# Performance work log

Measured on AMD Instinct MI355X. Metric: run time of the kernel, lower is better.

## Reference

```python
import jax, jax.numpy as jnp
import numpy as np

NUM_HEADS = 12

def setup_inputs() -> dict:
    key = jax.random.key(0)
    ks = jax.random.split(key, 9)
    B, N, C = 4, 1024, 768
    hd = C // NUM_HEADS  # 64
    return {
        "x": jax.random.normal(ks[0], (B, N, C), dtype=jnp.float32),
        "prev_attn": jax.random.uniform(ks[1], (B, NUM_HEADS, N, N), dtype=jnp.float32) / N,
        "qkv_w": jax.random.normal(ks[2], (3 * C, C), dtype=jnp.float32) * 0.02,
        "proj_w": jax.random.normal(ks[3], (C, C), dtype=jnp.float32) * 0.02,
        "proj_b": jax.random.normal(ks[4], (C,), dtype=jnp.float32) * 0.02,
        "bp_w1": jax.random.normal(ks[5], (hd // 2, 2 * hd), dtype=jnp.float32) * 0.02,
        "bp_b1": jax.random.normal(ks[6], (hd // 2,), dtype=jnp.float32) * 0.02,
        "bp_w2": jax.random.normal(ks[7], (3, hd // 2), dtype=jnp.float32) * 0.02,
        "bp_b2": jax.random.normal(ks[8], (3,), dtype=jnp.float32) * 0.02,
    }

def reference(x, prev_attn, qkv_w, proj_w, proj_b, bp_w1, bp_b1, bp_w2, bp_b2):
    B, N, C = x.shape
    H = NUM_HEADS
    hd = C // H
    scale = hd ** -0.5
    # qkv projection: [B,N,3C] -> [3,B,H,N,hd]
    qkv = (x @ qkv_w.T).reshape(B, N, 3, H, hd).transpose(2, 0, 3, 1, 4)
    q, k, v = qkv[0], qkv[1], qkv[2]
    # scaled dot-product scores [B,H,N,N]
    attn_logits = jnp.einsum('bhnd,bhmd->bhnm', q, k) * scale
    cur_attn = jax.nn.softmax(attn_logits, axis=-1)
    # per-(b,h,n) bias MLP on concat(q,k): [B,H,N,2*hd] -> [B,H,N,3]
    qk = jnp.concatenate((q, k), axis=-1)
    h1 = jax.nn.relu(jnp.einsum('bhnd,od->bhno', qk, bp_w1) + bp_b1)
    bias = jnp.abs(jnp.einsum('bhno,po->bhnp', h1, bp_w2) + bp_b2)  # [B,H,N,3]
    # blend current attention, previous attention, and uniform term
    attn = (cur_attn * (1.0 + bias[..., 0:1])
            + prev_attn * bias[..., 1:2]
            - bias[..., 2:3] / N)
    out = jnp.einsum('bhnm,bhmd->bhnd', attn, v)  # [B,H,N,hd]
    out = out.transpose(0, 2, 1, 3).reshape(B, N, C)
    out = out @ proj_w.T + proj_b
    return (out, cur_attn)
```

## Files before the change

kernel.cpp:

```cpp
#include <hip/hip_runtime.h>

typedef __bf16 bf16_t;
typedef __bf16 bf16x8 __attribute__((ext_vector_type(8)));
typedef __bf16 bf16x4 __attribute__((ext_vector_type(4)));
typedef float f32x4 __attribute__((ext_vector_type(4)));

static constexpr int Bb = 4, Hh = 12, Nn = 1024, Cc = 768, HD = 64;
static constexpr int OUT0 = Bb * Nn * Cc;

__global__ __launch_bounds__(256) void convert_all(
    const float* __restrict__ x, const float* __restrict__ qw, const float* __restrict__ pw,
    bf16_t* __restrict__ xb, bf16_t* __restrict__ qwb, bf16_t* __restrict__ pwb) {
  const int NX = (Bb * Nn * Cc) / 4;
  const int NQ = (3 * Cc * Cc) / 4;
  int i = blockIdx.x * 256 + threadIdx.x;
  const float4* src;
  bf16_t* dst;
  int off;
  if (i < NX) { src = (const float4*)x; dst = xb; off = i; }
  else if (i < NX + NQ) { src = (const float4*)qw; dst = qwb; off = i - NX; }
  else { src = (const float4*)pw; dst = pwb; off = i - NX - NQ; }
  float4 v = src[off];
  bf16x4 o;
  o[0] = (bf16_t)v.x; o[1] = (bf16_t)v.y; o[2] = (bf16_t)v.z; o[3] = (bf16_t)v.w;
  *(bf16x4*)(dst + (size_t)off * 4) = o;
}

template <int MODE>
__global__ __launch_bounds__(256) void gemm_bt(
    const bf16_t* __restrict__ A, const bf16_t* __restrict__ Bm, int N, int K,
    bf16_t* __restrict__ q_bf, bf16_t* __restrict__ k_bf, bf16_t* __restrict__ vT_bf,
    float* __restrict__ outF, const float* __restrict__ bias) {
  __shared__ bf16_t As[128 * 40];
  __shared__ bf16_t Bs[128 * 40];
  const int tid = threadIdx.x;
  const int lane = tid & 63;
  const int w = tid >> 6;
  const int wr = w >> 1, wc = w & 1;
  const int g = lane >> 4, r = lane & 15;
  const int ntiles = N >> 7;
  const int m0 = (blockIdx.x / ntiles) << 7;
  const int n0 = (blockIdx.x % ntiles) << 7;

  const f32x4 fz = {0.f, 0.f, 0.f, 0.f};
  f32x4 acc[4][4];
#pragma unroll
  for (int i = 0; i < 4; i++)
#pragma unroll
    for (int j = 0; j < 4; j++) acc[i][j] = fz;

  for (int k0 = 0; k0 < K; k0 += 32) {
#pragma unroll
    for (int p = 0; p < 2; p++) {
      int idx = tid + (p << 8);
      int row = idx >> 2;
      int kof = (idx & 3) << 3;
      *(bf16x8*)&As[row * 40 + kof] = *(const bf16x8*)&A[(size_t)(m0 + row) * K + k0 + kof];
      *(bf16x8*)&Bs[row * 40 + kof] = *(const bf16x8*)&Bm[(size_t)(n0 + row) * K + k0 + kof];
    }
    __syncthreads();
    bf16x8 af[4], bfv[4];
#pragma unroll
    for (int i = 0; i < 4; i++) af[i] = *(const bf16x8*)&As[(wr * 64 + i * 16 + r) * 40 + g * 8];
#pragma unroll
    for (int j = 0; j < 4; j++) bfv[j] = *(const bf16x8*)&Bs[(wc * 64 + j * 16 + r) * 40 + g * 8];
#pragma unroll
    for (int i = 0; i < 4; i++)
#pragma unroll
      for (int j = 0; j < 4; j++)
        acc[i][j] = __builtin_amdgcn_mfma_f32_16x16x32_bf16(af[i], bfv[j], acc[i][j], 0, 0, 0);
    __syncthreads();
  }

#pragma unroll
  for (int i = 0; i < 4; i++) {
#pragma unroll
    for (int j = 0; j < 4; j++) {
      int c = n0 + wc * 64 + j * 16 + r;
#pragma unroll
      for (int e = 0; e < 4; e++) {
        int mrow = m0 + wr * 64 + i * 16 + g * 4 + e;
        float val = acc[i][j][e];
        if constexpr (MODE == 0) {
          int which = c / 768;
          int cc = c - which * 768;
          int h = cc >> 6, d = cc & 63;
          int b = mrow >> 10, n = mrow & 1023;
          size_t bh = (size_t)(b * Hh + h);
          if (which == 0)      q_bf[(bh * Nn + n) * HD + d] = (bf16_t)val;
          else if (which == 1) k_bf[(bh * Nn + n) * HD + d] = (bf16_t)val;
          else                 vT_bf[(bh * HD + d) * Nn + n] = (bf16_t)val;
        } else {
          outF[(size_t)mrow * N + c] = val + bias[c];
        }
      }
    }
  }
}

__global__ __launch_bounds__(256) void bias_mlp(
    const bf16_t* __restrict__ qb, const bf16_t* __restrict__ kb,
    const float* __restrict__ w1, const float* __restrict__ b1,
    const float* __restrict__ w2, const float* __restrict__ b2,
    float* __restrict__ bias4) {
  __shared__ float w1s[32 * 129];
  __shared__ float qks[8][128];
  __shared__ float h1s[8][32];
  const int t = threadIdx.x;
#pragma unroll
  for (int p = 0; p < 16; p++) {
    int idx = p * 256 + t;
    w1s[(idx >> 7) * 129 + (idx & 127)] = w1[idx];
  }
  const int rl = t >> 5, u = t & 31;
  const int rowg = blockIdx.x * 8 + rl;
  {
    int i4 = u * 4;
    const bf16_t* src = (i4 < 64) ? (qb + (size_t)rowg * HD + i4)
                                  : (kb + (size_t)rowg * HD + (i4 - 64));
    bf16x4 vv = *(const bf16x4*)src;
#pragma unroll
    for (int z = 0; z < 4; z++) qks[rl][i4 + z] = (float)vv[z];
  }
  __syncthreads();
  float accv = b1[u];
#pragma unroll 8
  for (int i = 0; i < 128; i++) accv += qks[rl][i] * w1s[u * 129 + i];
  h1s[rl][u] = fmaxf(accv, 0.f);
  __syncthreads();
  if (u < 4) {
    float outv = 0.f;
    if (u < 3) {
      float s = b2[u];
#pragma unroll
      for (int j = 0; j < 32; j++) s += w2[u * 32 + j] * h1s[rl][j];
      float v = fabsf(s);
      outv = (u == 0) ? (1.f + v) : ((u == 1) ? v : -v * (1.f / (float)Nn));
    }
    bias4[(size_t)rowg * 4 + u] = outv;
  }
}

__global__ __launch_bounds__(256) void attn_fused(
    const bf16_t* __restrict__ qb, const bf16_t* __restrict__ kb,
    const bf16_t* __restrict__ vT, const float* __restrict__ prev,
    const float* __restrict__ bias4, float* __restrict__ cur,
    bf16_t* __restrict__ oh) {
  __shared__ bf16_t Pb[16 * 1024];
  __shared__ float redmax[16][4];
  __shared__ float redsum[16][4];
  const int bid = blockIdx.x;
  const int bh = bid >> 6, mt = bid & 63;
  const int tid = threadIdx.x;
  const int lane = tid & 63, w = tid >> 6;
  const int g = lane >> 4, r = lane & 15;
  const int row0 = mt << 4;

  const bf16_t* qp = qb + ((size_t)bh * Nn + row0) * HD;
  const bf16_t* kp = kb + (size_t)bh * Nn * HD;
  bf16x8 a0 = *(const bf16x8*)&qp[r * HD + g * 8];
  bf16x8 a1 = *(const bf16x8*)&qp[r * HD + g * 8 + 32];
  const f32x4 fz = {0.f, 0.f, 0.f, 0.f};
  f32x4 acc[16];
#pragma unroll
  for (int t = 0; t < 16; t++) {
    int col = (w << 8) + (t << 4) + r;
    bf16x8 b0 = *(const bf16x8*)&kp[(size_t)col * HD + g * 8];
    bf16x8 b1 = *(const bf16x8*)&kp[(size_t)col * HD + g * 8 + 32];
    f32x4 z = __builtin_amdgcn_mfma_f32_16x16x32_bf16(a0, b0, fz, 0, 0, 0);
    acc[t] = __builtin_amdgcn_mfma_f32_16x16x32_bf16(a1, b1, z, 0, 0, 0);
  }
  const float scale = 0.125f;
  float mj[4] = {-3.0e38f, -3.0e38f, -3.0e38f, -3.0e38f};
#pragma unroll
  for (int t = 0; t < 16; t++)
#pragma unroll
    for (int e = 0; e < 4; e++) {
      acc[t][e] *= scale;
      mj[e] = fmaxf(mj[e], acc[t][e]);
    }
#pragma unroll
  for (int s = 1; s < 16; s <<= 1)
#pragma unroll
    for (int e = 0; e < 4; e++) mj[e] = fmaxf(mj[e], __shfl_xor(mj[e], s, 64));
  if (r == 0) {
#pragma unroll
    for (int e = 0; e < 4; e++) redmax[g * 4 + e][w] = mj[e];
  }
  __syncthreads();
  float rm[4];
#pragma unroll
  for (int e = 0; e < 4; e++) {
    float v = fmaxf(redmax[g * 4 + e][0], redmax[g * 4 + e][1]);
    rm[e] = fmaxf(v, fmaxf(redmax[g * 4 + e][2], redmax[g * 4 + e][3]));
  }
  float sj[4] = {0.f, 0.f, 0.f, 0.f};
#pragma unroll
  for (int t = 0; t < 16; t++)
#pragma unroll
    for (int e = 0; e < 4; e++) {
      float ev = __expf(acc[t][e] - rm[e]);
      acc[t][e] = ev;
      sj[e] += ev;
    }
#pragma unroll
  for (int s = 1; s < 16; s <<= 1)
#pragma unroll
    for (int e = 0; e < 4; e++) sj[e] += __shfl_xor(sj[e], s, 64);
  if (r == 0) {
#pragma unroll
    for (int e = 0; e < 4; e++) redsum[g * 4 + e][w] = sj[e];
  }
  __syncthreads();
  float inv[4];
#pragma unroll
  for (int e = 0; e < 4; e++)
    inv[e] = 1.f / (redsum[g * 4 + e][0] + redsum[g * 4 + e][1] +
                    redsum[g * 4 + e][2] + redsum[g * 4 + e][3]);
  float* op = cur + (size_t)bh * Nn * Nn;
#pragma unroll
  for (int t = 0; t < 16; t++) {
    int col = (w << 8) + (t << 4) + r;
#pragma unroll
    for (int e = 0; e < 4; e++) {
      float p = acc[t][e] * inv[e];
      int row = g * 4 + e;
      op[(size_t)(row0 + row) * Nn + col] = p;
      Pb[row * 1024 + (col ^ ((row & 7) << 3))] = (bf16_t)p;
    }
  }
  __syncthreads();

  const float* pp = prev + (size_t)bh * Nn * Nn + (size_t)row0 * Nn;
  const float* bp = bias4 + ((size_t)(bh << 10) + row0) * 4;
#pragma unroll
  for (int i = 0; i < 16; i++) {
    float4 pv = *(const float4*)&pp[(size_t)i * Nn + tid * 4];
    float4 bv = *(const float4*)&bp[i * 4];
    int ci = (tid * 4) ^ ((i & 7) << 3);
    bf16x4 pbv = *(bf16x4*)&Pb[i * 1024 + ci];
    bf16x4 nb;
    nb[0] = (bf16_t)(bv.x * (float)pbv[0] + bv.y * pv.x + bv.z);
    nb[1] = (bf16_t)(bv.x * (float)pbv[1] + bv.y * pv.y + bv.z);
    nb[2] = (bf16_t)(bv.x * (float)pbv[2] + bv.y * pv.z + bv.z);
    nb[3] = (bf16_t)(bv.x * (float)pbv[3] + bv.y * pv.w + bv.z);
    *(bf16x4*)&Pb[i * 1024 + ci] = nb;
  }
  __syncthreads();

  const bf16_t* vp = vT + ((size_t)bh * HD + (w << 4) + r) * Nn;
  f32x4 c0 = fz, c1 = fz, c2 = fz, c3 = fz;
#pragma unroll
  for (int ks = 0; ks < 8; ks++) {
    int kA = ks * 32;
    bf16x8 afA = *(bf16x8*)&Pb[r * 1024 + ((kA + g * 8) ^ ((r & 7) << 3))];
    bf16x8 afB = *(bf16x8*)&Pb[r * 1024 + ((256 + kA + g * 8) ^ ((r & 7) << 3))];
    bf16x8 afC = *(bf16x8*)&Pb[r * 1024 + ((512 + kA + g * 8) ^ ((r & 7) << 3))];
    bf16x8 afD = *(bf16x8*)&Pb[r * 1024 + ((768 + kA + g * 8) ^ ((r & 7) << 3))];
    bf16x8 bA = *(const bf16x8*)&vp[kA + g * 8];
    bf16x8 bB = *(const bf16x8*)&vp[256 + kA + g * 8];
    bf16x8 bC = *(const bf16x8*)&vp[512 + kA + g * 8];
    bf16x8 bD = *(const bf16x8*)&vp[768 + kA + g * 8];
    c0 = __builtin_amdgcn_mfma_f32_16x16x32_bf16(afA, bA, c0, 0, 0, 0);
    c1 = __builtin_amdgcn_mfma_f32_16x16x32_bf16(afB, bB, c1, 0, 0, 0);
    c2 = __builtin_amdgcn_mfma_f32_16x16x32_bf16(afC, bC, c2, 0, 0, 0);
    c3 = __builtin_amdgcn_mfma_f32_16x16x32_bf16(afD, bD, c3, 0, 0, 0);
  }
  f32x4 osum = (c0 + c1) + (c2 + c3);
  const int b = bh / Hh, h = bh % Hh;
#pragma unroll
  for (int e = 0; e < 4; e++) {
    int nrow = row0 + g * 4 + e;
    oh[((size_t)(b * Nn + nrow)) * Cc + h * HD + (w << 4) + r] = (bf16_t)osum[e];
  }
}

extern "C" void kernel_launch(void* const* d_in, const int* in_sizes, int n_in,
                              void* d_out, int out_size, void* d_ws, size_t ws_size,
                              hipStream_t stream) {
  const float* x      = (const float*)d_in[0];
  const float* prev   = (const float*)d_in[1];
  const float* qkv_w  = (const float*)d_in[2];
  const float* proj_w = (const float*)d_in[3];
  const float* proj_b = (const float*)d_in[4];
  const float* bp_w1  = (const float*)d_in[5];
  const float* bp_b1  = (const float*)d_in[6];
  const float* bp_w2  = (const float*)d_in[7];
  const float* bp_w2b = (const float*)d_in[8];

  float* out0 = (float*)d_out;
  float* cur  = out0 + OUT0;

  char* ws = (char*)d_ws;
  bf16_t* xb    = (bf16_t*)(ws + 0);
  bf16_t* qwb   = (bf16_t*)(ws + 6291456);
  bf16_t* pwb   = (bf16_t*)(ws + 9830400);
  bf16_t* qbf   = (bf16_t*)(ws + 11010048);
  bf16_t* kbf   = (bf16_t*)(ws + 17301504);
  bf16_t* vtb   = (bf16_t*)(ws + 23592960);
  float*  bias4 = (float*)(ws + 29884416);
  bf16_t* ohb   = (bf16_t*)(ws + 30670848);
  if (ws_size < 36962304) return;

  convert_all<<<5376, 256, 0, stream>>>(x, qkv_w, proj_w, xb, qwb, pwb);
  gemm_bt<0><<<(4096 / 128) * (2304 / 128), 256, 0, stream>>>(
      xb, qwb, 2304, 768, qbf, kbf, vtb, nullptr, nullptr);
  bias_mlp<<<49152 / 8, 256, 0, stream>>>(qbf, kbf, bp_w1, bp_b1, bp_w2, bp_w2b, bias4);
  attn_fused<<<48 * 64, 256, 0, stream>>>(qbf, kbf, vtb, prev, bias4, cur, ohb);
  gemm_bt<1><<<(4096 / 128) * (768 / 128), 256, 0, stream>>>(
      ohb, pwb, 768, 768, nullptr, nullptr, nullptr, out0, proj_b);
}
```

Baseline: 249.1 us.

## Use direct global-to-LDS loads in QKV GEMM and restructure attention softmax stores

```diff
diff --git a/kernel.cpp b/kernel.cpp
--- a/kernel.cpp
+++ b/kernel.cpp
@@ -7,6 +7,11 @@
 
 static constexpr int Bb = 4, Hh = 12, Nn = 1024, Cc = 768, HD = 64;
 static constexpr int OUT0 = Bb * Nn * Cc;
+
+#define GLD16(gp, lp)                                                       \
+  __builtin_amdgcn_global_load_lds(                                         \
+      (const __attribute__((address_space(1))) unsigned int*)(gp),          \
+      (__attribute__((address_space(3))) unsigned int*)(lp), 16, 0, 0)
 
 __global__ __launch_bounds__(256) void convert_all(
     const float* __restrict__ x, const float* __restrict__ qw, const float* __restrict__ pw,
@@ -26,10 +31,73 @@
   *(bf16x4*)(dst + (size_t)off * 4) = o;
 }
 
+__global__ __launch_bounds__(256) void gemm_qkv(
+    const bf16_t* __restrict__ A, const bf16_t* __restrict__ Bm,
+    bf16_t* __restrict__ q_bf, bf16_t* __restrict__ k_bf, bf16_t* __restrict__ vT_bf) {
+  __shared__ bf16_t As[128 * 32];
+  __shared__ bf16_t Bs[128 * 32];
+  const int tid = threadIdx.x;
+  const int lane = tid & 63;
+  const int w = tid >> 6;
+  const int wr = w >> 1, wc = w & 1;
+  const int g = lane >> 4, r = lane & 15;
+  const int m0 = (blockIdx.x / 18) << 7;
+  const int n0 = (blockIdx.x % 18) << 7;
+
+  const f32x4 fz = {0.f, 0.f, 0.f, 0.f};
+  f32x4 acc[4][4];
+#pragma unroll
+  for (int i = 0; i < 4; i++)
+#pragma unroll
+    for (int j = 0; j < 4; j++) acc[i][j] = fz;
+
+  for (int k0 = 0; k0 < 768; k0 += 32) {
+#pragma unroll
+    for (int c = 0; c < 2; c++) {
+      int row = w * 32 + c * 16 + (lane >> 2);
+      int kof = (lane & 3) << 3;
+      GLD16(&A[(size_t)(m0 + row) * 768 + k0 + kof], (char*)As + w * 2048 + c * 1024);
+      GLD16(&Bm[(size_t)(n0 + row) * 768 + k0 + kof], (char*)Bs + w * 2048 + c * 1024);
+    }
+    __syncthreads();
+    bf16x8 af[4], bfv[4];
+#pragma unroll
+    for (int i = 0; i < 4; i++) af[i] = *(const bf16x8*)&As[(wr * 64 + i * 16 + r) * 32 + g * 8];
+#pragma unroll
+    for (int j = 0; j < 4; j++) bfv[j] = *(const bf16x8*)&Bs[(wc * 64 + j * 16 + r) * 32 + g * 8];
+#pragma unroll
+    for (int i = 0; i < 4; i++)
+#pragma unroll
+      for (int j = 0; j < 4; j++)
+        acc[i][j] = __builtin_amdgcn_mfma_f32_16x16x32_bf16(af[i], bfv[j], acc[i][j], 0, 0, 0);
+    __syncthreads();
+  }
+
+#pragma unroll
+  for (int i = 0; i < 4; i++) {
+#pragma unroll
+    for (int j = 0; j < 4; j++) {
+      int c = n0 + wc * 64 + j * 16 + r;
+#pragma unroll
+      for (int e = 0; e < 4; e++) {
+        int mrow = m0 + wr * 64 + i * 16 + g * 4 + e;
+        float val = acc[i][j][e];
+        int which = c / 768;
+        int cc = c - which * 768;
+        int h = cc >> 6, d = cc & 63;
+        int b = mrow >> 10, n = mrow & 1023;
+        size_t bh = (size_t)(b * Hh + h);
+        if (which == 0)      q_bf[(bh * Nn + n) * HD + d] = (bf16_t)val;
+        else if (which == 1) k_bf[(bh * Nn + n) * HD + d] = (bf16_t)val;
+        else                 vT_bf[(bh * HD + d) * Nn + n] = (bf16_t)val;
+      }
+    }
+  }
+}
+
 template <int MODE>
 __global__ __launch_bounds__(256) void gemm_bt(
     const bf16_t* __restrict__ A, const bf16_t* __restrict__ Bm, int N, int K,
-    bf16_t* __restrict__ q_bf, bf16_t* __restrict__ k_bf, bf16_t* __restrict__ vT_bf,
     float* __restrict__ outF, const float* __restrict__ bias) {
   __shared__ bf16_t As[128 * 40];
   __shared__ bf16_t Bs[128 * 40];
@@ -80,19 +148,7 @@
 #pragma unroll
       for (int e = 0; e < 4; e++) {
         int mrow = m0 + wr * 64 + i * 16 + g * 4 + e;
-        float val = acc[i][j][e];
-        if constexpr (MODE == 0) {
-          int which = c / 768;
-          int cc = c - which * 768;
-          int h = cc >> 6, d = cc & 63;
-          int b = mrow >> 10, n = mrow & 1023;
-          size_t bh = (size_t)(b * Hh + h);
-          if (which == 0)      q_bf[(bh * Nn + n) * HD + d] = (bf16_t)val;
-          else if (which == 1) k_bf[(bh * Nn + n) * HD + d] = (bf16_t)val;
-          else                 vT_bf[(bh * HD + d) * Nn + n] = (bf16_t)val;
-        } else {
-          outF[(size_t)mrow * N + c] = val + bias[c];
-        }
+        outF[(size_t)mrow * N + c] = acc[i][j][e] + bias[c];
       }
     }
   }
@@ -141,16 +197,17 @@
   }
 }
 
-__global__ __launch_bounds__(256) void attn_fused(
+__global__ __launch_bounds__(256, 4) void attn_fused(
     const bf16_t* __restrict__ qb, const bf16_t* __restrict__ kb,
     const bf16_t* __restrict__ vT, const float* __restrict__ prev,
     const float* __restrict__ bias4, float* __restrict__ cur,
     bf16_t* __restrict__ oh) {
-  __shared__ bf16_t Pb[16 * 1024];
+  __shared__ char Plb[16 * 2048];
   __shared__ float redmax[16][4];
   __shared__ float redsum[16][4];
   const int bid = blockIdx.x;
-  const int bh = bid >> 6, mt = bid & 63;
+  const int tile = (bid & 7) * 384 + (bid >> 3);
+  const int bh = tile >> 6, mt = tile & 63;
   const int tid = threadIdx.x;
   const int lane = tid & 63, w = tid >> 6;
   const int g = lane >> 4, r = lane & 15;
@@ -217,54 +274,64 @@
   for (int e = 0; e < 4; e++)
     inv[e] = 1.f / (redsum[g * 4 + e][0] + redsum[g * 4 + e][1] +
                     redsum[g * 4 + e][2] + redsum[g * 4 + e][3]);
-  float* op = cur + (size_t)bh * Nn * Nn;
 #pragma unroll
   for (int t = 0; t < 16; t++) {
     int col = (w << 8) + (t << 4) + r;
 #pragma unroll
     for (int e = 0; e < 4; e++) {
-      float p = acc[t][e] * inv[e];
       int row = g * 4 + e;
-      op[(size_t)(row0 + row) * Nn + col] = p;
-      Pb[row * 1024 + (col ^ ((row & 7) << 3))] = (bf16_t)p;
-    }
-  }
-  __syncthreads();
-
-  const float* pp = prev + (size_t)bh * Nn * Nn + (size_t)row0 * Nn;
+      int off = (row * 2048 + col * 2) ^ ((row & 7) << 4);
+      *(bf16_t*)(Plb + off) = (bf16_t)(acc[t][e] * inv[e]);
+    }
+  }
+  __syncthreads();
+
+  const int c4 = tid << 2;
+  const float* pp = prev + (size_t)bh * Nn * Nn + (size_t)row0 * Nn + c4;
+  float* cp = cur + (size_t)bh * Nn * Nn + (size_t)row0 * Nn + c4;
   const float* bp = bias4 + ((size_t)(bh << 10) + row0) * 4;
 #pragma unroll
-  for (int i = 0; i < 16; i++) {
-    float4 pv = *(const float4*)&pp[(size_t)i * Nn + tid * 4];
-    float4 bv = *(const float4*)&bp[i * 4];
-    int ci = (tid * 4) ^ ((i & 7) << 3);
-    bf16x4 pbv = *(bf16x4*)&Pb[i * 1024 + ci];
-    bf16x4 nb;
-    nb[0] = (bf16_t)(bv.x * (float)pbv[0] + bv.y * pv.x + bv.z);
-    nb[1] = (bf16_t)(bv.x * (float)pbv[1] + bv.y * pv.y + bv.z);
-    nb[2] = (bf16_t)(bv.x * (float)pbv[2] + bv.y * pv.z + bv.z);
-    nb[3] = (bf16_t)(bv.x * (float)pbv[3] + bv.y * pv.w + bv.z);
-    *(bf16x4*)&Pb[i * 1024 + ci] = nb;
-  }
-  __syncthreads();
-
-  const bf16_t* vp = vT + ((size_t)bh * HD + (w << 4) + r) * Nn;
+  for (int half = 0; half < 2; half++) {
+    float4 pv[8];
+#pragma unroll
+    for (int i = 0; i < 8; i++)
+      pv[i] = *(const float4*)&pp[(size_t)(half * 8 + i) * Nn];
+#pragma unroll
+    for (int i = 0; i < 8; i++) {
+      int row = half * 8 + i;
+      int off = (row * 2048 + c4 * 2) ^ ((row & 7) << 4);
+      bf16x4 p4 = *(const bf16x4*)(Plb + off);
+      float4 pf;
+      pf.x = (float)p4[0]; pf.y = (float)p4[1]; pf.z = (float)p4[2]; pf.w = (float)p4[3];
+      *(float4*)&cp[(size_t)row * Nn] = pf;
+      float4 bv = *(const float4*)&bp[row * 4];
+      bf16x4 nb;
+      nb[0] = (bf16_t)(bv.x * pf.x + bv.y * pv[i].x + bv.z);
+      nb[1] = (bf16_t)(bv.x * pf.y + bv.y * pv[i].y + bv.z);
+      nb[2] = (bf16_t)(bv.x * pf.z + bv.y * pv[i].z + bv.z);
+      nb[3] = (bf16_t)(bv.x * pf.w + bv.y * pv[i].w + bv.z);
+      *(bf16x4*)(Plb + off) = nb;
+    }
+  }
+  __syncthreads();
+
+  const bf16_t* vrow = vT + (size_t)bh * HD * Nn + (size_t)((w << 4) + r) * Nn;
   f32x4 c0 = fz, c1 = fz, c2 = fz, c3 = fz;
 #pragma unroll
   for (int ks = 0; ks < 8; ks++) {
-    int kA = ks * 32;
-    bf16x8 afA = *(bf16x8*)&Pb[r * 1024 + ((kA + g * 8) ^ ((r & 7) << 3))];
-    bf16x8 afB = *(bf16x8*)&Pb[r * 1024 + ((256 + kA + g * 8) ^ ((r & 7) << 3))];
-    bf16x8 afC = *(bf16x8*)&Pb[r * 1024 + ((512 + kA + g * 8) ^ ((r & 7) << 3))];
-    bf16x8 afD = *(bf16x8*)&Pb[r * 1024 + ((768 + kA + g * 8) ^ ((r & 7) << 3))];
-    bf16x8 bA = *(const bf16x8*)&vp[kA + g * 8];
-    bf16x8 bB = *(const bf16x8*)&vp[256 + kA + g * 8];
-    bf16x8 bC = *(const bf16x8*)&vp[512 + kA + g * 8];
-    bf16x8 bD = *(const bf16x8*)&vp[768 + kA + g * 8];
-    c0 = __builtin_amdgcn_mfma_f32_16x16x32_bf16(afA, bA, c0, 0, 0, 0);
-    c1 = __builtin_amdgcn_mfma_f32_16x16x32_bf16(afB, bB, c1, 0, 0, 0);
-    c2 = __builtin_amdgcn_mfma_f32_16x16x32_bf16(afC, bC, c2, 0, 0, 0);
-    c3 = __builtin_amdgcn_mfma_f32_16x16x32_bf16(afD, bD, c3, 0, 0, 0);
+    int kA = ks << 5;
+    bf16x8 pA = *(const bf16x8*)(Plb + ((r * 2048 + (kA + g * 8) * 2) ^ ((r & 7) << 4)));
+    bf16x8 pB = *(const bf16x8*)(Plb + ((r * 2048 + (256 + kA + g * 8) * 2) ^ ((r & 7) << 4)));
+    bf16x8 pC = *(const bf16x8*)(Plb + ((r * 2048 + (512 + kA + g * 8) * 2) ^ ((r & 7) << 4)));
+    bf16x8 pD = *(const bf16x8*)(Plb + ((r * 2048 + (768 + kA + g * 8) * 2) ^ ((r & 7) << 4)));
+    bf16x8 vA = *(const bf16x8*)&vrow[kA + g * 8];
+    bf16x8 vB = *(const bf16x8*)&vrow[256 + kA + g * 8];
+    bf16x8 vC = *(const bf16x8*)&vrow[512 + kA + g * 8];
+    bf16x8 vD = *(const bf16x8*)&vrow[768 + kA + g * 8];
+    c0 = __builtin_amdgcn_mfma_f32_16x16x32_bf16(pA, vA, c0, 0, 0, 0);
+    c1 = __builtin_amdgcn_mfma_f32_16x16x32_bf16(pB, vB, c1, 0, 0, 0);
+    c2 = __builtin_amdgcn_mfma_f32_16x16x32_bf16(pC, vC, c2, 0, 0, 0);
+    c3 = __builtin_amdgcn_mfma_f32_16x16x32_bf16(pD, vD, c3, 0, 0, 0);
   }
   f32x4 osum = (c0 + c1) + (c2 + c3);
   const int b = bh / Hh, h = bh % Hh;
@@ -303,10 +370,9 @@
   if (ws_size < 36962304) return;
 
   convert_all<<<5376, 256, 0, stream>>>(x, qkv_w, proj_w, xb, qwb, pwb);
-  gemm_bt<0><<<(4096 / 128) * (2304 / 128), 256, 0, stream>>>(
-      xb, qwb, 2304, 768, qbf, kbf, vtb, nullptr, nullptr);
+  gemm_qkv<<<32 * 18, 256, 0, stream>>>(xb, qwb, qbf, kbf, vtb);
   bias_mlp<<<49152 / 8, 256, 0, stream>>>(qbf, kbf, bp_w1, bp_b1, bp_w2, bp_w2b, bias4);
-  attn_fused<<<48 * 64, 256, 0, stream>>>(qbf, kbf, vtb, prev, bias4, cur, ohb);
+  attn_fused<<<3072, 256, 0, stream>>>(qbf, kbf, vtb, prev, bias4, cur, ohb);
   gemm_bt<1><<<(4096 / 128) * (768 / 128), 256, 0, stream>>>(
-      ohb, pwb, 768, 768, nullptr, nullptr, nullptr, out0, proj_b);
-}
+      ohb, pwb, 768, 768, out0, proj_b);
+}
```

Result: faster. 240.9 us (-3.3%).
